# Kernel tuning notes

Measured on AMD Instinct MI355X. Metric: run time of the kernel, lower is better.

The kernel has to match this reference:

```python
import jax, jax.numpy as jnp
import numpy as np

NDIM = 128
DEPTH = 6
NPASSES = 4
N_NODES = 50000
N_EDGES = 800000
NODE_IN = 5
LN_EPS = 1e-5


def _mlp_params(key, depth, ndim):
    ks = jax.random.split(key, 6)
    s = 0.05
    return dict(
        W1=jax.random.normal(ks[0], (depth, ndim, ndim), jnp.float32) * s,
        b1=jnp.zeros((depth, ndim), jnp.float32),
        W2=jax.random.normal(ks[1], (depth, ndim, ndim), jnp.float32) * s,
        b2=jnp.zeros((depth, ndim), jnp.float32),
        g=jnp.ones((depth, ndim), jnp.float32),
        bt=jnp.zeros((depth, ndim), jnp.float32),
    )


def setup_inputs() -> dict:
    key = jax.random.key(0)
    k = jax.random.split(key, 8)
    v = jax.random.normal(k[0], (1, N_NODES, NODE_IN), jnp.float32)
    ij = jax.random.randint(k[1], (2, N_EDGES), 0, N_NODES, dtype=jnp.int64)
    ep = _mlp_params(k[2], DEPTH, NDIM)
    npar = _mlp_params(k[3], DEPTH, NDIM)
    return {
        'v': v, 'ij': ij,
        'enc_W': jax.random.normal(k[4], (NODE_IN, NDIM), jnp.float32) * 0.05,
        'enc_b': jnp.zeros((NDIM,), jnp.float32),
        'edge_W1': ep['W1'], 'edge_b1': ep['b1'], 'edge_W2': ep['W2'], 'edge_b2': ep['b2'],
        'edge_g': ep['g'], 'edge_bt': ep['bt'],
        'node_W1': npar['W1'], 'node_b1': npar['b1'], 'node_W2': npar['W2'], 'node_b2': npar['b2'],
        'node_g': npar['g'], 'node_bt': npar['bt'],
        'dec_W': jax.random.normal(k[5], (NDIM, NODE_IN), jnp.float32) * 0.05,
        'dec_b': jnp.zeros((NODE_IN,), jnp.float32),
    }


def _res_block(x, W1, b1, W2, b2, g, bt):
    # x + LayerNorm(relu(relu(x W1 + b1) W2 + b2)); dropout is identity (eval)
    h = jax.nn.relu(x @ W1 + b1)
    h = jax.nn.relu(h @ W2 + b2)
    mu = jnp.mean(h, axis=-1, keepdims=True)
    var = jnp.var(h, axis=-1, keepdims=True)
    h = (h - mu) * jax.lax.rsqrt(var + LN_EPS) * g + bt
    return x + h


def _mlp(x, W1, b1, W2, b2, g, bt):
    for i in range(W1.shape[0]):
        x = _res_block(x, W1[i], b1[i], W2[i], b2[i], g[i], bt[i])
    return x


def reference(v, ij, enc_W, enc_b,
              edge_W1, edge_b1, edge_W2, edge_b2, edge_g, edge_bt,
              node_W1, node_b1, node_W2, node_b2, node_g, node_bt,
              dec_W, dec_b):
    ij0, ij1 = ij[0], ij[1]
    h = v @ enc_W + enc_b                      # [B, N, D]
    e = None
    for _ in range(NPASSES):
        # Edge update: gather endpoint features
        x = h[:, ij0] - h[:, ij1]              # [B, E, D]
        if e is not None:
            x = x + e
        e = _mlp(x, edge_W1, edge_b1, edge_W2, edge_b2, edge_g, edge_bt)
        # Node update: scatter-sum edges to destination nodes
        agg = jnp.zeros_like(h).at[:, ij1].add(e)
        h = _mlp(h + agg, node_W1, node_b1, node_W2, node_b2, node_g, node_bt)
    return h @ dec_W + dec_b                   # [B, N, node_input_dim]
```

## Files before the change

kernel.cpp:

```cpp
#include <hip/hip_runtime.h>
#include <hip/hip_bf16.h>
#include <cstdint>
#include <cstddef>

#define NDIMC   128
#define DEPTHC  6
#define NPASSESC 4
#define NNODES  50000
#define NEDGES  800000
#define NODEIN  5
#define LNEPS   1e-5f

#define H_OFF    0ull
#define E_OFF    25600000ull
#define PW_OFF   230400000ull
#define FLAG_OFF 231186432ull
#define DEG_OFF  231186436ull
#define RS_OFF   231386440ull
#define CUR_OFF  231586444ull
#define EIDX_OFF 231786444ull
#define PWMAT    98304

typedef __attribute__((ext_vector_type(8))) short mgn_sh8;
typedef __attribute__((ext_vector_type(4))) float mgn_f32x4;

__device__ __forceinline__ unsigned mgn_bf16bits(float f) {
    unsigned x = __float_as_uint(f);
    return (x + 0x7fffu + ((x >> 16) & 1u)) >> 16;
}
__device__ __forceinline__ unsigned mgn_pk(float a, float b) {
    __hip_bfloat162 t = __float22bfloat162_rn(make_float2(a, b));
    union { __hip_bfloat162 h; unsigned u; } c; c.h = t; return c.u;
}

__device__ __forceinline__ void mgn_cp16(const unsigned short* g, unsigned short* l) {
    __builtin_amdgcn_global_load_lds(
        (const __attribute__((address_space(1))) void*)g,
        (__attribute__((address_space(3))) void*)l, 16, 0, 0);
}
template <int BW>
__device__ __forceinline__ void mgn_stage_q(const unsigned short* __restrict__ src,
                                            unsigned short* wbuf, int tid) {
    const int w = tid >> 6, l = tid & 63;
#pragma unroll
    for (int i = 0; i < 8 / BW; ++i) {
        const int off = (w * (8 / BW) + i) * 512 + l * 8;
        mgn_cp16(src + off, wbuf + off);
    }
}

__device__ __forceinline__ void mgn_qcompN(const unsigned short* __restrict__ buf, int l,
                                           const mgn_sh8* a0p, const mgn_sh8* a1p,
                                           mgn_f32x4* acc0, mgn_f32x4* acc1) {
#pragma unroll
    for (int t = 0; t < 4; ++t)
#pragma unroll
        for (int sp = 0; sp < 2; ++sp) {
            mgn_sh8 b = *(const mgn_sh8*)&buf[(t * 2 + sp) * 512 + l * 8];
            acc0[t] = __builtin_amdgcn_mfma_f32_16x16x32_bf16(a0p[sp], b, acc0[t], 0, 0, 0);
            acc1[t] = __builtin_amdgcn_mfma_f32_16x16x32_bf16(a1p[sp], b, acc1[t], 0, 0, 0);
        }
}

__global__ void mgn_detect_kernel(const int* __restrict__ ij, int* __restrict__ flag) {
    __shared__ int any;
    if (threadIdx.x == 0) any = 0;
    __syncthreads();
    if (ij[2 * threadIdx.x + 1] != 0) atomicOr(&any, 1);
    __syncthreads();
    if (threadIdx.x == 0) *flag = any;
}

__device__ __forceinline__ long mgn_load_idx(const int* __restrict__ ij, long pos, int is32) {
    if (is32) return (long)ij[pos];
    const long long* ij8 = (const long long*)ij;
    return (long)ij8[pos];
}

__global__ void mgn_pack_kernel(const float* __restrict__ W, unsigned short* __restrict__ pw) {
    int i = blockIdx.x * blockDim.x + threadIdx.x;
    if (i >= PWMAT) return;
    int j    = i & 7;
    int lane = (i >> 3) & 63;
    int sp   = (i >> 9) & 1;
    int tp   = (i >> 10) & 3;
    int qd   = (i >> 12) & 3;
    int d    = i >> 14;
    int sh = qd & 1, nh = qd >> 1;
    int k = (sh * 2 + sp) * 32 + (lane >> 4) * 8 + j;
    int n = (lane & 15) * 8 + nh * 4 + tp;
    pw[i] = (unsigned short)mgn_bf16bits(W[(d * NDIMC + k) * NDIMC + n]);
}

__global__ void mgn_deg_kernel(const int* __restrict__ ij, const int* __restrict__ flag,
                               int* __restrict__ deg) {
    int e = blockIdx.x * blockDim.x + threadIdx.x;
    if (e >= NEDGES) return;
    int dst = (int)mgn_load_idx(ij, (long)NEDGES + e, *flag);
    atomicAdd(&deg[dst], 1);
}

__global__ void mgn_scan_kernel(const int* __restrict__ deg,
                                int* __restrict__ rowstart, int* __restrict__ cursor) {
    __shared__ int partial[256];
    const int tid = threadIdx.x;
    const int CH = (NNODES + 255) / 256;
    const int base = tid * CH;
    int s = 0;
    for (int i = 0; i < CH; ++i) {
        int idx = base + i;
        if (idx < NNODES) s += deg[idx];
    }
    partial[tid] = s;
    __syncthreads();
    for (int off = 1; off < 256; off <<= 1) {
        int add = (tid >= off) ? partial[tid - off] : 0;
        __syncthreads();
        partial[tid] += add;
        __syncthreads();
    }
    int run = (tid == 0) ? 0 : partial[tid - 1];
    for (int i = 0; i < CH; ++i) {
        int idx = base + i;
        if (idx < NNODES) {
            rowstart[idx] = run;
            cursor[idx]   = run;
            run += deg[idx];
        }
    }
    if (tid == 255) rowstart[NNODES] = run;
}

__global__ void mgn_fill_kernel(const int* __restrict__ ij, const int* __restrict__ flag,
                                int* __restrict__ cursor, int* __restrict__ eidx) {
    int e = blockIdx.x * blockDim.x + threadIdx.x;
    if (e >= NEDGES) return;
    int dst = (int)mgn_load_idx(ij, (long)NEDGES + e, *flag);
    int pos = atomicAdd(&cursor[dst], 1);
    eidx[pos] = e;
}

__global__ void mgn_encoder_kernel(const float* __restrict__ v,
                                   const float* __restrict__ encW,
                                   const float* __restrict__ encB,
                                   float* __restrict__ h) {
    int idx = blockIdx.x * blockDim.x + threadIdx.x;
    if (idx >= NNODES * NDIMC) return;
    int n = idx >> 7, d = idx & 127;
    float acc = encB[d];
#pragma unroll
    for (int k = 0; k < NODEIN; ++k)
        acc = fmaf(v[n * NODEIN + k], encW[k * NDIMC + d], acc);
    h[idx] = acc;
}

__global__ void mgn_decoder_kernel(const float* __restrict__ h,
                                   const float* __restrict__ decW,
                                   const float* __restrict__ decB,
                                   float* __restrict__ out) {
    int idx = blockIdx.x * blockDim.x + threadIdx.x;
    if (idx >= NNODES * NODEIN) return;
    int n = idx / NODEIN, j = idx % NODEIN;
    float acc = decB[j];
#pragma unroll 8
    for (int k = 0; k < NDIMC; ++k)
        acc = fmaf(h[n * NDIMC + k], decW[k * NODEIN + j], acc);
    out[idx] = acc;
}

template <int MODE, int BW>
__global__ __launch_bounds__(BW * 64, 3) void mgn_mlp6_mfma_kernel(
    float* __restrict__ Xf,
    unsigned short* __restrict__ Eb,
    const float* __restrict__ H,
    const int* __restrict__ ij,
    const int* __restrict__ flag,
    const int* __restrict__ rowstart,
    const int* __restrict__ eidx,
    int addE, int nrows,
    const unsigned short* __restrict__ PW1,
    const unsigned short* __restrict__ PW2,
    const float* __restrict__ B1, const float* __restrict__ B2,
    const float* __restrict__ G,  const float* __restrict__ BT)
{
    __shared__ unsigned short xl[BW * 32 * 136];
    __shared__ unsigned short wqA[4096];
    __shared__ unsigned short wqB[4096];
    const int tid = threadIdx.x;
    const int w   = tid >> 6;
    const int l   = tid & 63;
    const int q   = l >> 4;
    const int lm  = l & 15;
    const int ct  = lm * 8;
    const int wbase = w * 32;
    const long rowbase = (long)blockIdx.x * (32 * BW);

    const int is32 = (MODE == 1) ? *flag : 0;

    mgn_stage_q<BW>(PW1, wqA, tid);

    float xres[8][8];
#pragma unroll
    for (int rr = 0; rr < 8; ++rr) {
        const int rloc = wbase + (rr >> 2) * 16 + q * 4 + (rr & 3);
        long gr = rowbase + rloc;
        bool ok = gr < nrows;
        float xv[8];
#pragma unroll
        for (int t = 0; t < 8; ++t) xv[t] = 0.f;
        if (MODE == 1) {
            if (ok) {
                long er = (long)eidx[gr];
                long i0 = mgn_load_idx(ij, er, is32);
                long i1 = mgn_load_idx(ij, (long)NEDGES + er, is32);
                const float* p0 = H + i0 * NDIMC + ct;
                const float* p1 = H + i1 * NDIMC + ct;
                float4 a0 = *(const float4*)p0, a1 = *(const float4*)(p0 + 4);
                float4 b0 = *(const float4*)p1, b1 = *(const float4*)(p1 + 4);
                xv[0] = a0.x - b0.x; xv[1] = a0.y - b0.y;
                xv[2] = a0.z - b0.z; xv[3] = a0.w - b0.w;
                xv[4] = a1.x - b1.x; xv[5] = a1.y - b1.y;
                xv[6] = a1.z - b1.z; xv[7] = a1.w - b1.w;
                if (addE) {
                    uint4 u4 = *(const uint4*)(Eb + (size_t)gr * NDIMC + ct);
                    xv[0] += __uint_as_float(u4.x << 16);
                    xv[1] += __uint_as_float(u4.x & 0xffff0000u);
                    xv[2] += __uint_as_float(u4.y << 16);
                    xv[3] += __uint_as_float(u4.y & 0xffff0000u);
                    xv[4] += __uint_as_float(u4.z << 16);
                    xv[5] += __uint_as_float(u4.z & 0xffff0000u);
                    xv[6] += __uint_as_float(u4.w << 16);
                    xv[7] += __uint_as_float(u4.w & 0xffff0000u);
                }
            }
        } else {
            if (ok) {
                float4 a0 = *(const float4*)(Xf + gr * NDIMC + ct);
                float4 a1 = *(const float4*)(Xf + gr * NDIMC + ct + 4);
                xv[0] = a0.x; xv[1] = a0.y; xv[2] = a0.z; xv[3] = a0.w;
                xv[4] = a1.x; xv[5] = a1.y; xv[6] = a1.z; xv[7] = a1.w;
                int rs = rowstart[gr], re = rowstart[gr + 1];
                for (int k = rs; k < re; ++k) {
                    uint4 u4 = *(const uint4*)(Eb + (size_t)k * NDIMC + ct);
                    xv[0] += __uint_as_float(u4.x << 16);
                    xv[1] += __uint_as_float(u4.x & 0xffff0000u);
                    xv[2] += __uint_as_float(u4.y << 16);
                    xv[3] += __uint_as_float(u4.y & 0xffff0000u);
                    xv[4] += __uint_as_float(u4.z << 16);
                    xv[5] += __uint_as_float(u4.z & 0xffff0000u);
                    xv[6] += __uint_as_float(u4.w << 16);
                    xv[7] += __uint_as_float(u4.w & 0xffff0000u);
                }
            }
        }
#pragma unroll
        for (int t = 0; t < 8; ++t) xres[rr][t] = xv[t];
        uint4 pk;
        pk.x = mgn_pk(xv[0], xv[1]); pk.y = mgn_pk(xv[2], xv[3]);
        pk.z = mgn_pk(xv[4], xv[5]); pk.w = mgn_pk(xv[6], xv[7]);
        *(uint4*)&xl[rloc * 136 + ct] = pk;
    }

    __syncthreads();

    mgn_sh8 a0[4], a1[4];
    mgn_f32x4 acc0[4], acc1[4];
    const int arow0 = (wbase + lm) * 136;
    const int arow1 = (wbase + 16 + lm) * 136;

    for (int d = 0; d < DEPTHC; ++d) {
        const unsigned short* pw1 = PW1 + (size_t)d * 16384;
        const unsigned short* pw2 = PW2 + (size_t)d * 16384;

#pragma unroll
        for (int s = 0; s < 4; ++s) {
            a0[s] = *(const mgn_sh8*)&xl[arow0 + s * 32 + q * 8];
            a1[s] = *(const mgn_sh8*)&xl[arow1 + s * 32 + q * 8];
        }
        {
            float4 bb = *(const float4*)(B1 + d * NDIMC + ct);
            acc0[0] = (mgn_f32x4){bb.x, bb.x, bb.x, bb.x};
            acc0[1] = (mgn_f32x4){bb.y, bb.y, bb.y, bb.y};
            acc0[2] = (mgn_f32x4){bb.z, bb.z, bb.z, bb.z};
            acc0[3] = (mgn_f32x4){bb.w, bb.w, bb.w, bb.w};
            acc1[0] = acc0[0]; acc1[1] = acc0[1]; acc1[2] = acc0[2]; acc1[3] = acc0[3];
        }

        mgn_stage_q<BW>(pw1 + 4096, wqB, tid);
        mgn_qcompN(wqA, l, a0 + 0, a1 + 0, acc0, acc1);
        __syncthreads();
        mgn_stage_q<BW>(pw1 + 8192, wqA, tid);
        mgn_qcompN(wqB, l, a0 + 2, a1 + 2, acc0, acc1);
#pragma unroll
        for (int rr = 0; rr < 8; ++rr) {
            const int rloc = wbase + (rr >> 2) * 16 + q * 4 + (rr & 3);
            const int r = rr & 3;
            float v0 = fmaxf((rr < 4) ? acc0[0][r] : acc1[0][r], 0.f);
            float v1 = fmaxf((rr < 4) ? acc0[1][r] : acc1[1][r], 0.f);
            float v2 = fmaxf((rr < 4) ? acc0[2][r] : acc1[2][r], 0.f);
            float v3 = fmaxf((rr < 4) ? acc0[3][r] : acc1[3][r], 0.f);
            uint2 pk; pk.x = mgn_pk(v0, v1); pk.y = mgn_pk(v2, v3);
            *(uint2*)&xl[rloc * 136 + ct] = pk;
        }
        {
            float4 bb = *(const float4*)(B1 + d * NDIMC + ct + 4);
            acc0[0] = (mgn_f32x4){bb.x, bb.x, bb.x, bb.x};
            acc0[1] = (mgn_f32x4){bb.y, bb.y, bb.y, bb.y};
            acc0[2] = (mgn_f32x4){bb.z, bb.z, bb.z, bb.z};
            acc0[3] = (mgn_f32x4){bb.w, bb.w, bb.w, bb.w};
            acc1[0] = acc0[0]; acc1[1] = acc0[1]; acc1[2] = acc0[2]; acc1[3] = acc0[3];
        }
        __syncthreads();
        mgn_stage_q<BW>(pw1 + 12288, wqB, tid);
        mgn_qcompN(wqA, l, a0 + 0, a1 + 0, acc0, acc1);
        __syncthreads();
        mgn_stage_q<BW>(pw2, wqA, tid);
        mgn_qcompN(wqB, l, a0 + 2, a1 + 2, acc0, acc1);
#pragma unroll
        for (int rr = 0; rr < 8; ++rr) {
            const int rloc = wbase + (rr >> 2) * 16 + q * 4 + (rr & 3);
            const int r = rr & 3;
            float v0 = fmaxf((rr < 4) ? acc0[0][r] : acc1[0][r], 0.f);
            float v1 = fmaxf((rr < 4) ? acc0[1][r] : acc1[1][r], 0.f);
            float v2 = fmaxf((rr < 4) ? acc0[2][r] : acc1[2][r], 0.f);
            float v3 = fmaxf((rr < 4) ? acc0[3][r] : acc1[3][r], 0.f);
            uint2 pk; pk.x = mgn_pk(v0, v1); pk.y = mgn_pk(v2, v3);
            *(uint2*)&xl[rloc * 136 + ct + 4] = pk;
        }
#pragma unroll
        for (int s = 0; s < 4; ++s) {
            a0[s] = *(const mgn_sh8*)&xl[arow0 + s * 32 + q * 8];
            a1[s] = *(const mgn_sh8*)&xl[arow1 + s * 32 + q * 8];
        }
        {
            float4 bb = *(const float4*)(B2 + d * NDIMC + ct);
            acc0[0] = (mgn_f32x4){bb.x, bb.x, bb.x, bb.x};
            acc0[1] = (mgn_f32x4){bb.y, bb.y, bb.y, bb.y};
            acc0[2] = (mgn_f32x4){bb.z, bb.z, bb.z, bb.z};
            acc0[3] = (mgn_f32x4){bb.w, bb.w, bb.w, bb.w};
            acc1[0] = acc0[0]; acc1[1] = acc0[1]; acc1[2] = acc0[2]; acc1[3] = acc0[3];
        }
        __syncthreads();
        mgn_stage_q<BW>(pw2 + 4096, wqB, tid);
        mgn_qcompN(wqA, l, a0 + 0, a1 + 0, acc0, acc1);
        __syncthreads();
        mgn_stage_q<BW>(pw2 + 8192, wqA, tid);
        mgn_qcompN(wqB, l, a0 + 2, a1 + 2, acc0, acc1);
#pragma unroll
        for (int rr = 0; rr < 8; ++rr) {
            const int rloc = wbase + (rr >> 2) * 16 + q * 4 + (rr & 3);
            const int r = rr & 3;
            float v0 = fmaxf((rr < 4) ? acc0[0][r] : acc1[0][r], 0.f);
            float v1 = fmaxf((rr < 4) ? acc0[1][r] : acc1[1][r], 0.f);
            float v2 = fmaxf((rr < 4) ? acc0[2][r] : acc1[2][r], 0.f);
            float v3 = fmaxf((rr < 4) ? acc0[3][r] : acc1[3][r], 0.f);
            uint2 pk; pk.x = mgn_pk(v0, v1); pk.y = mgn_pk(v2, v3);
            *(uint2*)&xl[rloc * 136 + ct] = pk;
        }
        {
            float4 bb = *(const float4*)(B2 + d * NDIMC + ct + 4);
            acc0[0] = (mgn_f32x4){bb.x, bb.x, bb.x, bb.x};
            acc0[1] = (mgn_f32x4){bb.y, bb.y, bb.y, bb.y};
            acc0[2] = (mgn_f32x4){bb.z, bb.z, bb.z, bb.z};
            acc0[3] = (mgn_f32x4){bb.w, bb.w, bb.w, bb.w};
            acc1[0] = acc0[0]; acc1[1] = acc0[1]; acc1[2] = acc0[2]; acc1[3] = acc0[3];
        }
        __syncthreads();
        mgn_stage_q<BW>(pw2 + 12288, wqB, tid);
        mgn_qcompN(wqA, l, a0 + 0, a1 + 0, acc0, acc1);
        __syncthreads();
        if (d + 1 < DEPTHC)
            mgn_stage_q<BW>(PW1 + (size_t)(d + 1) * 16384, wqA, tid);
        mgn_qcompN(wqB, l, a0 + 2, a1 + 2, acc0, acc1);

        {
            float4 ga  = *(const float4*)(G  + d * NDIMC + ct);
            float4 gb  = *(const float4*)(G  + d * NDIMC + ct + 4);
            float4 bta = *(const float4*)(BT + d * NDIMC + ct);
            float4 btb = *(const float4*)(BT + d * NDIMC + ct + 4);
            float gv[8]  = {ga.x, ga.y, ga.z, ga.w, gb.x, gb.y, gb.z, gb.w};
            float btv[8] = {bta.x, bta.y, bta.z, bta.w, btb.x, btb.y, btb.z, btb.w};
#pragma unroll
            for (int rr = 0; rr < 8; ++rr) {
                const int rloc = wbase + (rr >> 2) * 16 + q * 4 + (rr & 3);
                const int r = rr & 3;
                float h2[8];
                uint2 st = *(const uint2*)&xl[rloc * 136 + ct];
                h2[0] = __uint_as_float(st.x << 16);
                h2[1] = __uint_as_float(st.x & 0xffff0000u);
                h2[2] = __uint_as_float(st.y << 16);
                h2[3] = __uint_as_float(st.y & 0xffff0000u);
#pragma unroll
                for (int t = 0; t < 4; ++t)
                    h2[4 + t] = fmaxf((rr < 4) ? acc0[t][r] : acc1[t][r], 0.f);
                float sum = 0.f, ssq = 0.f;
#pragma unroll
                for (int t = 0; t < 8; ++t) {
                    sum += h2[t];
                    ssq = fmaf(h2[t], h2[t], ssq);
                }
                sum += __shfl_xor(sum, 1); ssq += __shfl_xor(ssq, 1);
                sum += __shfl_xor(sum, 2); ssq += __shfl_xor(ssq, 2);
                sum += __shfl_xor(sum, 4); ssq += __shfl_xor(ssq, 4);
                sum += __shfl_xor(sum, 8); ssq += __shfl_xor(ssq, 8);
                float mean = sum * 0.0078125f;
                float var  = fmaf(-mean, mean, ssq * 0.0078125f);
                float rstd = rsqrtf(var + LNEPS);
#pragma unroll
                for (int t = 0; t < 8; ++t) {
                    float at = rstd * gv[t];
                    float ctt = fmaf(-mean, at, btv[t]);
                    xres[rr][t] += fmaf(h2[t], at, ctt);
                }
                if (d != DEPTHC - 1) {
                    uint4 pk;
                    pk.x = mgn_pk(xres[rr][0], xres[rr][1]);
                    pk.y = mgn_pk(xres[rr][2], xres[rr][3]);
                    pk.z = mgn_pk(xres[rr][4], xres[rr][5]);
                    pk.w = mgn_pk(xres[rr][6], xres[rr][7]);
                    *(uint4*)&xl[rloc * 136 + ct] = pk;
                }
            }
        }
        if (d + 1 < DEPTHC) __syncthreads();
    }

#pragma unroll
    for (int rr = 0; rr < 8; ++rr) {
        const int rloc = wbase + (rr >> 2) * 16 + q * 4 + (rr & 3);
        long gr = rowbase + rloc;
        if (gr < nrows) {
            if (MODE == 1) {
                uint4 pk;
                pk.x = mgn_pk(xres[rr][0], xres[rr][1]);
                pk.y = mgn_pk(xres[rr][2], xres[rr][3]);
                pk.z = mgn_pk(xres[rr][4], xres[rr][5]);
                pk.w = mgn_pk(xres[rr][6], xres[rr][7]);
                *(uint4*)(Eb + (size_t)gr * NDIMC + ct) = pk;
            } else {
                float4 o0 = {xres[rr][0], xres[rr][1], xres[rr][2], xres[rr][3]};
                float4 o1 = {xres[rr][4], xres[rr][5], xres[rr][6], xres[rr][7]};
                *(float4*)(Xf + gr * NDIMC + ct)     = o0;
                *(float4*)(Xf + gr * NDIMC + ct + 4) = o1;
            }
        }
    }
}

extern "C" void kernel_launch(void* const* d_in, const int* in_sizes, int n_in,
                              void* d_out, int out_size, void* d_ws, size_t ws_size,
                              hipStream_t stream) {
    const float* v    = (const float*)d_in[0];
    const int*   ij   = (const int*)d_in[1];
    const float* encW = (const float*)d_in[2];
    const float* encB = (const float*)d_in[3];
    const float* eW1  = (const float*)d_in[4];
    const float* eB1  = (const float*)d_in[5];
    const float* eW2  = (const float*)d_in[6];
    const float* eB2  = (const float*)d_in[7];
    const float* eG   = (const float*)d_in[8];
    const float* eBT  = (const float*)d_in[9];
    const float* nW1  = (const float*)d_in[10];
    const float* nB1  = (const float*)d_in[11];
    const float* nW2  = (const float*)d_in[12];
    const float* nB2  = (const float*)d_in[13];
    const float* nG   = (const float*)d_in[14];
    const float* nBT  = (const float*)d_in[15];
    const float* decW = (const float*)d_in[16];
    const float* decB = (const float*)d_in[17];
    float* out = (float*)d_out;

    char* ws = (char*)d_ws;
    float*          h    = (float*)(ws + H_OFF);
    unsigned short* ebuf = (unsigned short*)(ws + E_OFF);
    unsigned short* pw   = (unsigned short*)(ws + PW_OFF);
    int*            flag = (int*)(ws + FLAG_OFF);
    int*            deg  = (int*)(ws + DEG_OFF);
    int*            rstt = (int*)(ws + RS_OFF);
    int*            curs = (int*)(ws + CUR_OFF);
    int*            eidx = (int*)(ws + EIDX_OFF);

    mgn_detect_kernel<<<1, 256, 0, stream>>>(ij, flag);
    mgn_pack_kernel<<<(PWMAT + 255) / 256, 256, 0, stream>>>(eW1, pw + 0 * PWMAT);
    mgn_pack_kernel<<<(PWMAT + 255) / 256, 256, 0, stream>>>(eW2, pw + 1 * PWMAT);
    mgn_pack_kernel<<<(PWMAT + 255) / 256, 256, 0, stream>>>(nW1, pw + 2 * PWMAT);
    mgn_pack_kernel<<<(PWMAT + 255) / 256, 256, 0, stream>>>(nW2, pw + 3 * PWMAT);

    hipMemsetAsync(deg, 0, (size_t)(NNODES + 1) * sizeof(int), stream);
    mgn_deg_kernel<<<(NEDGES + 255) / 256, 256, 0, stream>>>(ij, flag, deg);
    mgn_scan_kernel<<<1, 256, 0, stream>>>(deg, rstt, curs);
    mgn_fill_kernel<<<(NEDGES + 255) / 256, 256, 0, stream>>>(ij, flag, curs, eidx);

    mgn_encoder_kernel<<<(NNODES * NDIMC + 255) / 256, 256, 0, stream>>>(v, encW, encB, h);

    for (int p = 0; p < NPASSESC; ++p) {
        mgn_mlp6_mfma_kernel<1, 4><<<NEDGES / 128, 256, 0, stream>>>(
            nullptr, ebuf, h, ij, flag, nullptr, eidx, p > 0 ? 1 : 0, NEDGES,
            pw + 0 * PWMAT, pw + 1 * PWMAT, eB1, eB2, eG, eBT);
        mgn_mlp6_mfma_kernel<0, 4><<<(NNODES + 127) / 128, 256, 0, stream>>>(
            h, ebuf, nullptr, nullptr, nullptr, rstt, nullptr, 0, NNODES,
            pw + 2 * PWMAT, pw + 3 * PWMAT, nB1, nB2, nG, nBT);
    }

    mgn_decoder_kernel<<<(NNODES * NODEIN + 255) / 256, 256, 0, stream>>>(h, decW, decB, out);
}
```

Measured before the change: 3.200 ms.

## Swizzle LDS activation tile, keep layer-2 half in registers, use DPP reductions

Replaces the padded 136-stride LDS activation tile with an unpadded 128-stride layout whose columns are XOR-swizzled by row, removing bank conflicts while shrinking LDS use. The first half of the second GEMM's ReLU output is kept packed in registers rather than written to and reread from LDS. Part of the LayerNorm cross-lane reduction switches from shuffles to DPP row operations, and MFMA loops raise wave priority with s_setprio. Holding more values in registers may raise VGPR pressure under the 3-block launch bound.

```diff
diff --git a/kernel.cpp b/kernel.cpp
--- a/kernel.cpp
+++ b/kernel.cpp
@@ -33,6 +33,16 @@
     union { __hip_bfloat162 h; unsigned u; } c; c.h = t; return c.u;
 }
 
+__device__ __forceinline__ int mgn_xli(int row, int colsh) {
+    return row * 128 + (colsh ^ ((row & 7) << 3));
+}
+
+template <int CTRL>
+__device__ __forceinline__ float mgn_dppadd(float x) {
+    int y = __builtin_amdgcn_update_dpp(0, __float_as_int(x), CTRL, 0xF, 0xF, true);
+    return x + __int_as_float(y);
+}
+
 __device__ __forceinline__ void mgn_cp16(const unsigned short* g, unsigned short* l) {
     __builtin_amdgcn_global_load_lds(
         (const __attribute__((address_space(1))) void*)g,
@@ -52,6 +62,7 @@
 __device__ __forceinline__ void mgn_qcompN(const unsigned short* __restrict__ buf, int l,
                                            const mgn_sh8* a0p, const mgn_sh8* a1p,
                                            mgn_f32x4* acc0, mgn_f32x4* acc1) {
+    __builtin_amdgcn_s_setprio(1);
 #pragma unroll
     for (int t = 0; t < 4; ++t)
 #pragma unroll
@@ -60,6 +71,7 @@
             acc0[t] = __builtin_amdgcn_mfma_f32_16x16x32_bf16(a0p[sp], b, acc0[t], 0, 0, 0);
             acc1[t] = __builtin_amdgcn_mfma_f32_16x16x32_bf16(a1p[sp], b, acc1[t], 0, 0, 0);
         }
+    __builtin_amdgcn_s_setprio(0);
 }
 
 __global__ void mgn_detect_kernel(const int* __restrict__ ij, int* __restrict__ flag) {
@@ -183,7 +195,7 @@
     const float* __restrict__ B1, const float* __restrict__ B2,
     const float* __restrict__ G,  const float* __restrict__ BT)
 {
-    __shared__ unsigned short xl[BW * 32 * 136];
+    __shared__ unsigned short xl[BW * 32 * 128];
     __shared__ unsigned short wqA[4096];
     __shared__ unsigned short wqB[4096];
     const int tid = threadIdx.x;
@@ -258,15 +270,16 @@
         uint4 pk;
         pk.x = mgn_pk(xv[0], xv[1]); pk.y = mgn_pk(xv[2], xv[3]);
         pk.z = mgn_pk(xv[4], xv[5]); pk.w = mgn_pk(xv[6], xv[7]);
-        *(uint4*)&xl[rloc * 136 + ct] = pk;
+        *(uint4*)&xl[mgn_xli(rloc, ct)] = pk;
     }
 
     __syncthreads();
 
     mgn_sh8 a0[4], a1[4];
     mgn_f32x4 acc0[4], acc1[4];
-    const int arow0 = (wbase + lm) * 136;
-    const int arow1 = (wbase + 16 + lm) * 136;
+    unsigned h2st[8][2];
+    const int rowA0 = wbase + lm;
+    const int rowA1 = wbase + 16 + lm;
 
     for (int d = 0; d < DEPTHC; ++d) {
         const unsigned short* pw1 = PW1 + (size_t)d * 16384;
@@ -274,8 +287,8 @@
 
 #pragma unroll
         for (int s = 0; s < 4; ++s) {
-            a0[s] = *(const mgn_sh8*)&xl[arow0 + s * 32 + q * 8];
-            a1[s] = *(const mgn_sh8*)&xl[arow1 + s * 32 + q * 8];
+            a0[s] = *(const mgn_sh8*)&xl[mgn_xli(rowA0, s * 32 + q * 8)];
+            a1[s] = *(const mgn_sh8*)&xl[mgn_xli(rowA1, s * 32 + q * 8)];
         }
         {
             float4 bb = *(const float4*)(B1 + d * NDIMC + ct);
@@ -300,7 +313,7 @@
             float v2 = fmaxf((rr < 4) ? acc0[2][r] : acc1[2][r], 0.f);
             float v3 = fmaxf((rr < 4) ? acc0[3][r] : acc1[3][r], 0.f);
             uint2 pk; pk.x = mgn_pk(v0, v1); pk.y = mgn_pk(v2, v3);
-            *(uint2*)&xl[rloc * 136 + ct] = pk;
+            *(uint2*)&xl[mgn_xli(rloc, ct)] = pk;
         }
         {
             float4 bb = *(const float4*)(B1 + d * NDIMC + ct + 4);
@@ -325,12 +338,12 @@
             float v2 = fmaxf((rr < 4) ? acc0[2][r] : acc1[2][r], 0.f);
             float v3 = fmaxf((rr < 4) ? acc0[3][r] : acc1[3][r], 0.f);
             uint2 pk; pk.x = mgn_pk(v0, v1); pk.y = mgn_pk(v2, v3);
-            *(uint2*)&xl[rloc * 136 + ct + 4] = pk;
+            *(uint2*)&xl[mgn_xli(rloc, ct + 4)] = pk;
         }
 #pragma unroll
         for (int s = 0; s < 4; ++s) {
-            a0[s] = *(const mgn_sh8*)&xl[arow0 + s * 32 + q * 8];
-            a1[s] = *(const mgn_sh8*)&xl[arow1 + s * 32 + q * 8];
+            a0[s] = *(const mgn_sh8*)&xl[mgn_xli(rowA0, s * 32 + q * 8)];
+            a1[s] = *(const mgn_sh8*)&xl[mgn_xli(rowA1, s * 32 + q * 8)];
         }
         {
             float4 bb = *(const float4*)(B2 + d * NDIMC + ct);
@@ -348,14 +361,13 @@
         mgn_qcompN(wqB, l, a0 + 2, a1 + 2, acc0, acc1);
 #pragma unroll
         for (int rr = 0; rr < 8; ++rr) {
-            const int rloc = wbase + (rr >> 2) * 16 + q * 4 + (rr & 3);
             const int r = rr & 3;
             float v0 = fmaxf((rr < 4) ? acc0[0][r] : acc1[0][r], 0.f);
             float v1 = fmaxf((rr < 4) ? acc0[1][r] : acc1[1][r], 0.f);
             float v2 = fmaxf((rr < 4) ? acc0[2][r] : acc1[2][r], 0.f);
             float v3 = fmaxf((rr < 4) ? acc0[3][r] : acc1[3][r], 0.f);
-            uint2 pk; pk.x = mgn_pk(v0, v1); pk.y = mgn_pk(v2, v3);
-            *(uint2*)&xl[rloc * 136 + ct] = pk;
+            h2st[rr][0] = mgn_pk(v0, v1);
+            h2st[rr][1] = mgn_pk(v2, v3);
         }
         {
             float4 bb = *(const float4*)(B2 + d * NDIMC + ct + 4);
@@ -385,11 +397,10 @@
                 const int rloc = wbase + (rr >> 2) * 16 + q * 4 + (rr & 3);
                 const int r = rr & 3;
                 float h2[8];
-                uint2 st = *(const uint2*)&xl[rloc * 136 + ct];
-                h2[0] = __uint_as_float(st.x << 16);
-                h2[1] = __uint_as_float(st.x & 0xffff0000u);
-                h2[2] = __uint_as_float(st.y << 16);
-                h2[3] = __uint_as_float(st.y & 0xffff0000u);
+                h2[0] = __uint_as_float(h2st[rr][0] << 16);
+                h2[1] = __uint_as_float(h2st[rr][0] & 0xffff0000u);
+                h2[2] = __uint_as_float(h2st[rr][1] << 16);
+                h2[3] = __uint_as_float(h2st[rr][1] & 0xffff0000u);
 #pragma unroll
                 for (int t = 0; t < 4; ++t)
                     h2[4 + t] = fmaxf((rr < 4) ? acc0[t][r] : acc1[t][r], 0.f);
@@ -399,10 +410,10 @@
                     sum += h2[t];
                     ssq = fmaf(h2[t], h2[t], ssq);
                 }
-                sum += __shfl_xor(sum, 1); ssq += __shfl_xor(ssq, 1);
-                sum += __shfl_xor(sum, 2); ssq += __shfl_xor(ssq, 2);
-                sum += __shfl_xor(sum, 4); ssq += __shfl_xor(ssq, 4);
-                sum += __shfl_xor(sum, 8); ssq += __shfl_xor(ssq, 8);
+                sum = mgn_dppadd<0xB1>(sum);  ssq = mgn_dppadd<0xB1>(ssq);
+                sum = mgn_dppadd<0x4E>(sum);  ssq = mgn_dppadd<0x4E>(ssq);
+                sum += __shfl_xor(sum, 4);    ssq += __shfl_xor(ssq, 4);
+                sum = mgn_dppadd<0x128>(sum); ssq = mgn_dppadd<0x128>(ssq);
                 float mean = sum * 0.0078125f;
                 float var  = fmaf(-mean, mean, ssq * 0.0078125f);
                 float rstd = rsqrtf(var + LNEPS);
@@ -418,7 +429,7 @@
                     pk.y = mgn_pk(xres[rr][2], xres[rr][3]);
                     pk.z = mgn_pk(xres[rr][4], xres[rr][5]);
                     pk.w = mgn_pk(xres[rr][6], xres[rr][7]);
-                    *(uint4*)&xl[rloc * 136 + ct] = pk;
+                    *(uint4*)&xl[mgn_xli(rloc, ct)] = pk;
                 }
             }
         }
```

Result: slower. 5.068 ms (+58.4%).
